# Performance work log

Hardware: AMD Instinct MI355X
Metric: run time of the kernel (lower is better)

Reference implementation:

```python
import jax, jax.numpy as jnp
import numpy as np

V, D, L, H, T_BLK, DFF = 50257, 768, 12, 12, 1024, 4096
DK = D // H
LN_EPS = 1e-5


def setup_inputs() -> dict:
    key = jax.random.key(0)
    ks = jax.random.split(key, 16)
    s = 0.02
    inp = {
        "idx": jax.random.randint(ks[0], (2, 1024), 0, V),
        "tok_emb": jax.random.normal(ks[1], (V, D), jnp.float32) * s,
        "pos_emb": jax.random.normal(ks[2], (1, T_BLK, D), jnp.float32) * s,
        "ln1_w": jnp.ones((L, D), jnp.float32),
        "ln1_b": jnp.zeros((L, D), jnp.float32),
        "qkv_w": jax.random.normal(ks[3], (L, 3 * D, D), jnp.float32) * s,
        "qkv_b": jnp.zeros((L, 3 * D), jnp.float32),
        "proj_w": jax.random.normal(ks[4], (L, D, D), jnp.float32) * s,
        "proj_b": jnp.zeros((L, D), jnp.float32),
        "ln2_w": jnp.ones((L, D), jnp.float32),
        "ln2_b": jnp.zeros((L, D), jnp.float32),
        "ff1_w": jax.random.normal(ks[5], (L, DFF, D), jnp.float32) * s,
        "ff1_b": jnp.zeros((L, DFF), jnp.float32),
        "ff2_w": jax.random.normal(ks[6], (L, D, DFF), jnp.float32) * s,
        "ff2_b": jnp.zeros((L, D), jnp.float32),
        "lnf_w": jnp.ones((D,), jnp.float32),
        "lnf_b": jnp.zeros((D,), jnp.float32),
        "head_w": jax.random.normal(ks[7], (V, D), jnp.float32) * s,
    }
    return inp


def _layernorm(x, w, b):
    mu = jnp.mean(x, axis=-1, keepdims=True)
    var = jnp.var(x, axis=-1, keepdims=True)
    return (x - mu) * jax.lax.rsqrt(var + LN_EPS) * w + b


def _gpt_forward(idx, tok_emb, pos_emb, ln1_w, ln1_b, qkv_w, qkv_b, proj_w, proj_b,
                 ln2_w, ln2_b, ff1_w, ff1_b, ff2_w, ff2_b, lnf_w, lnf_b, head_w):
    B, T = idx.shape
    x = tok_emb[idx] + pos_emb[:, :T, :]  # [B,T,D]
    mask = jnp.tril(jnp.ones((T, T), bool))  # causal
    scale = 1.0 / np.sqrt(DK)

    def step(x, p):
        l1w, l1b, qw, qb, pw, pb, l2w, l2b, f1w, f1b, f2w, f2b = p
        h = _layernorm(x, l1w, l1b)
        qkv = h @ qw.T + qb  # [B,T,3D]
        q, k, v = jnp.split(qkv, 3, axis=-1)
        q = q.reshape(B, T, H, DK).transpose(0, 2, 1, 3)  # [B,H,T,DK]
        k = k.reshape(B, T, H, DK).transpose(0, 2, 1, 3)
        v = v.reshape(B, T, H, DK).transpose(0, 2, 1, 3)
        att = jnp.einsum('bhtd,bhsd->bhts', q, k) * scale
        att = jnp.where(mask, att, -jnp.inf)
        att = jax.nn.softmax(att, axis=-1)
        y = jnp.einsum('bhts,bhsd->bhtd', att, v)
        y = y.transpose(0, 2, 1, 3).reshape(B, T, D)
        x = x + y @ pw.T + pb
        h2 = _layernorm(x, l2w, l2b)
        ff = jax.nn.gelu(h2 @ f1w.T + f1b, approximate=False) @ f2w.T + f2b
        return x + ff, None

    params = (ln1_w, ln1_b, qkv_w, qkv_b, proj_w, proj_b,
              ln2_w, ln2_b, ff1_w, ff1_b, ff2_w, ff2_b)
    x, _ = jax.lax.scan(step, x, params)
    x = _layernorm(x, lnf_w, lnf_b)
    return x @ head_w.T  # [B,T,V] logits


def reference(idx, tok_emb, pos_emb, ln1_w, ln1_b, qkv_w, qkv_b, proj_w, proj_b,
              ln2_w, ln2_b, ff1_w, ff1_b, ff2_w, ff2_b, lnf_w, lnf_b, head_w):
    return _gpt_forward(idx, tok_emb, pos_emb, ln1_w, ln1_b, qkv_w, qkv_b, proj_w,
                        proj_b, ln2_w, ln2_b, ff1_w, ff1_b, ff2_w, ff2_b,
                        lnf_w, lnf_b, head_w)
```

## Files before the change

### kernel.cpp

```cpp
#include <hip/hip_runtime.h>
#include <hip/hip_bf16.h>
#include <math.h>

#define Dm 768
#define Tt 1024
#define Bb 2
#define Hh 12
#define DFF 4096
#define Ll 12
#define Vv 50257
#define ROWS (Bb*Tt)
#define LN_EPS 1e-5f

typedef unsigned int uint;
typedef unsigned short ushort;
typedef float f32x4 __attribute__((ext_vector_type(4)));
typedef short bf16x8 __attribute__((ext_vector_type(8)));
typedef ushort us8 __attribute__((ext_vector_type(8)));

__device__ __forceinline__ ushort f2bf(float f) {
  uint u = __builtin_bit_cast(uint, f);
  u += 0x7FFFu + ((u >> 16) & 1u);
  return (ushort)(u >> 16);
}

#define GLL(gp, lp)                                                          \
  __builtin_amdgcn_global_load_lds(                                          \
      (const __attribute__((address_space(1))) uint*)(gp),                   \
      (__attribute__((address_space(3))) uint*)(lp), 16, 0, 0)

#define MF(a, b, c) __builtin_amdgcn_mfma_f32_16x16x32_bf16(a, b, c, 0, 0, 0)

__global__ __launch_bounds__(256) void embed_ln(
    const int* __restrict__ idx, const float* __restrict__ tok,
    const float* __restrict__ pos, const float* __restrict__ w,
    const float* __restrict__ b, float* __restrict__ x,
    ushort* __restrict__ out) {
  const int row = blockIdx.x;
  const int t = row & (Tt - 1);
  const int tid = threadIdx.x;
  const float* tsrc = tok + (size_t)idx[row] * Dm;
  const float* psrc = pos + (size_t)t * Dm;
  float v[3];
  float sum = 0.f, sq = 0.f;
#pragma unroll
  for (int i = 0; i < 3; i++) {
    const int d = tid + i * 256;
    v[i] = tsrc[d] + psrc[d];
    x[(size_t)row * Dm + d] = v[i];
    sum += v[i]; sq += v[i] * v[i];
  }
#pragma unroll
  for (int off = 32; off > 0; off >>= 1) {
    sum += __shfl_xor(sum, off);
    sq  += __shfl_xor(sq, off);
  }
  __shared__ float red[8];
  const int wid = tid >> 6, lane = tid & 63;
  if (lane == 0) { red[wid] = sum; red[wid + 4] = sq; }
  __syncthreads();
  sum = red[0] + red[1] + red[2] + red[3];
  sq  = red[4] + red[5] + red[6] + red[7];
  const float mu = sum * (1.f / Dm);
  const float var = sq * (1.f / Dm) - mu * mu;
  const float rstd = rsqrtf(var + LN_EPS);
  ushort* dst = out + (size_t)row * Dm;
#pragma unroll
  for (int i = 0; i < 3; i++) {
    const int d = tid + i * 256;
    dst[d] = f2bf((v[i] - mu) * rstd * w[d] + b[d]);
  }
}

__global__ __launch_bounds__(192) void red_ln(
    const float* __restrict__ part, int nsk, const float* __restrict__ bias,
    float* __restrict__ x, const float* __restrict__ w,
    const float* __restrict__ b, ushort* __restrict__ out) {
  const int row = blockIdx.x;
  const int tid = threadIdx.x;
  const size_t o4 = (size_t)row * 192 + tid;
  float4 xv = ((const float4*)x)[o4];
  const float4 b4 = ((const float4*)bias)[tid];
  xv.x += b4.x; xv.y += b4.y; xv.z += b4.z; xv.w += b4.w;
  for (int k = 0; k < nsk; k++) {
    const float4 p = ((const float4*)part)[(size_t)k * ROWS * 192 + o4];
    xv.x += p.x; xv.y += p.y; xv.z += p.z; xv.w += p.w;
  }
  ((float4*)x)[o4] = xv;
  float sum = xv.x + xv.y + xv.z + xv.w;
  float sq = xv.x * xv.x + xv.y * xv.y + xv.z * xv.z + xv.w * xv.w;
#pragma unroll
  for (int off = 32; off > 0; off >>= 1) {
    sum += __shfl_xor(sum, off);
    sq  += __shfl_xor(sq, off);
  }
  __shared__ float red[6];
  const int wid = tid >> 6, lane = tid & 63;
  if (lane == 0) { red[wid] = sum; red[wid + 3] = sq; }
  __syncthreads();
  sum = red[0] + red[1] + red[2];
  sq  = red[3] + red[4] + red[5];
  const float mu = sum * (1.f / Dm);
  const float var = sq * (1.f / Dm) - mu * mu;
  const float rstd = rsqrtf(var + LN_EPS);
  const float4 w4 = ((const float4*)w)[tid];
  const float4 bb4 = ((const float4*)b)[tid];
  ushort4 o;
  o.x = f2bf((xv.x - mu) * rstd * w4.x + bb4.x);
  o.y = f2bf((xv.y - mu) * rstd * w4.y + bb4.y);
  o.z = f2bf((xv.z - mu) * rstd * w4.z + bb4.z);
  o.w = f2bf((xv.w - mu) * rstd * w4.w + bb4.w);
  ((ushort4*)out)[o4] = o;
}

__global__ __launch_bounds__(256) void convert_w(
    const float* __restrict__ s, ushort* __restrict__ d, int n4) {
  const int stride = gridDim.x * 256;
  for (int i = blockIdx.x * 256 + threadIdx.x; i < n4; i += stride) {
    const float4 v = ((const float4*)s)[i];
    ushort4 o;
    o.x = f2bf(v.x); o.y = f2bf(v.y); o.z = f2bf(v.z); o.w = f2bf(v.w);
    ((ushort4*)d)[i] = o;
  }
}

#define EPI_QKV 0
#define EPI_PART 1
#define EPI_BIAS_GELU 2
#define EPI_NONE 3

template <int EPI>
__global__ __launch_bounds__(256) void gemm_mfma(
    const ushort* __restrict__ A, const ushort* __restrict__ B,
    const float* __restrict__ bias, void* __restrict__ Cv,
    void* __restrict__ Cv2, int Kloop, int Kstr, int Nloc, int ldC) {
  __shared__ char lds[32768];
  const int tid = threadIdx.x;
  const int l = tid & 63;
  const int wid = __builtin_amdgcn_readfirstlane(tid >> 6);
  const int wr = wid >> 1, wc = wid & 1;
  const int m0 = blockIdx.y * 128;
  const int n0 = blockIdx.x * 128;
  const int z = (EPI == EPI_PART) ? blockIdx.z : 0;
  if (EPI == EPI_PART) { A += (size_t)z * Kloop; B += (size_t)z * Kloop; }

  const int cperm = (((l & 3) ^ ((l >> 3) & 3)) * 8);
  const ushort* gA = A + (size_t)(m0 + wid * 32 + (l >> 2)) * Kstr + cperm;
  int rB = n0 + wid * 32 + (l >> 2);
  rB = min(rB, Nloc - 1);
  const ushort* gB = B + (size_t)rB * Kstr + cperm;

  const int rdSw = (l & 15) * 64 + (((l >> 4) ^ ((l >> 1) & 3)) * 16);
  const int aRd = wr * 4096 + rdSw;
  const int bRd = 8192 + wc * 4096 + rdSw;

  f32x4 acc[4][4] = {};
  const int nt = Kloop / 32;

  {
    const int lb = wid * 2048;
    GLL(gA, lds + lb);          GLL(gA + 16 * Kstr, lds + lb + 1024);
    GLL(gB, lds + 8192 + lb);   GLL(gB + 16 * Kstr, lds + 8192 + lb + 1024);
  }

  for (int t = 0; t < nt; ++t) {
    __syncthreads();
    if (t + 1 < nt) {
      const int base = ((t + 1) & 1) * 16384;
      const int lb = base + wid * 2048;
      const ushort* a = gA + (t + 1) * 32;
      const ushort* b = gB + (t + 1) * 32;
      GLL(a, lds + lb);         GLL(a + 16 * Kstr, lds + lb + 1024);
      GLL(b, lds + 8192 + lb);  GLL(b + 16 * Kstr, lds + 8192 + lb + 1024);
    }
    const int base = (t & 1) * 16384;
    bf16x8 av[4], bv[4];
#pragma unroll
    for (int i = 0; i < 4; ++i) {
      av[i] = *(const bf16x8*)(lds + base + aRd + i * 1024);
      bv[i] = *(const bf16x8*)(lds + base + bRd + i * 1024);
    }
#pragma unroll
    for (int i = 0; i < 4; ++i)
#pragma unroll
      for (int j = 0; j < 4; ++j)
        acc[i][j] = MF(av[i], bv[j], acc[i][j]);
  }

#pragma unroll
  for (int fm = 0; fm < 4; ++fm) {
    const int row0 = m0 + wr * 64 + fm * 16 + (l >> 4) * 4;
#pragma unroll
    for (int fn = 0; fn < 4; ++fn) {
      const int col = n0 + wc * 64 + fn * 16 + (l & 15);
      if (col >= Nloc) continue;
      float bi = 0.f;
      if (EPI == EPI_QKV || EPI == EPI_BIAS_GELU) bi = bias[col];
      if (EPI == EPI_QKV && col >= 2 * Dm) {
        const int hh = (col - 2 * Dm) >> 6, dd = col & 63;
        const int bI = row0 >> 10, t0 = row0 & (Tt - 1);
        ushort4 o4;
        o4.x = f2bf(acc[fm][fn][0] + bi);
        o4.y = f2bf(acc[fm][fn][1] + bi);
        o4.z = f2bf(acc[fm][fn][2] + bi);
        o4.w = f2bf(acc[fm][fn][3] + bi);
        *(ushort4*)((ushort*)Cv2 +
                    ((size_t)((bI * Hh + hh) * 64 + dd)) * Tt + t0) = o4;
        continue;
      }
#pragma unroll
      for (int r = 0; r < 4; ++r) {
        float v = acc[fm][fn][r] + bi;
        const size_t off = (size_t)(row0 + r) * ldC + col;
        if (EPI == EPI_BIAS_GELU) {
          v = 0.5f * v * (1.f + erff(v * 0.70710678118654752f));
          ((ushort*)Cv)[off] = f2bf(v);
        } else if (EPI == EPI_QKV) {
          ((ushort*)Cv)[off] = f2bf(v);
        } else if (EPI == EPI_PART) {
          ((float*)Cv)[(size_t)z * ROWS * ldC + off] = v;
        } else {
          ((float*)Cv)[off] = v;
        }
      }
    }
  }
}

__global__ __launch_bounds__(512, 2) void gemm_head8(
    const ushort* __restrict__ A, const ushort* __restrict__ B,
    float* __restrict__ C) {
  __shared__ char lds[131072];
  const int tid = threadIdx.x;
  const int l = tid & 63;
  const int wid = __builtin_amdgcn_readfirstlane(tid >> 6);
  const int wm = wid >> 2, wn = wid & 3;
  const int s = l & 15, g = l >> 4;

  const int bid = blockIdx.x;
  const int swz = (bid & 7) * 197 + (bid >> 3);
  const int pan = swz >> 3, mrw = swz & 7;
  const int m0 = mrw * 256;
  const int n0 = pan * 256;

  const int r0 = tid >> 3;
  const int q0 = (tid & 7) ^ (r0 & 7);
  const ushort* pA0 = A + (size_t)(m0 + r0) * Dm + q0 * 8;
  const ushort* pA1 = pA0 + (size_t)64 * Dm;
  const ushort* pB[2][2];
  pB[0][0] = B + (size_t)min(n0 + r0, Vv - 1) * Dm + q0 * 8;
  pB[0][1] = B + (size_t)min(n0 + 64 + r0, Vv - 1) * Dm + q0 * 8;
  pB[1][0] = B + (size_t)min(n0 + 128 + r0, Vv - 1) * Dm + q0 * 8;
  pB[1][1] = B + (size_t)min(n0 + 192 + r0, Vv - 1) * Dm + q0 * 8;

#define STG_A(t, h) do { if ((t) < 12) {                                     \
    char* _d = lds + ((((t) & 1) * 2 + (h)) * 16384);                        \
    GLL(pA0 + (size_t)(h) * 98304 + (t) * 64, _d + tid * 16);                \
    GLL(pA1 + (size_t)(h) * 98304 + (t) * 64, _d + 8192 + tid * 16);         \
  }} while (0)
#define STG_B(t, h) do { if ((t) < 12) {                                     \
    char* _d = lds + 65536 + ((((t) & 1) * 2 + (h)) * 16384);                \
    GLL(pB[h][0] + (t) * 64, _d + tid * 16);                                 \
    GLL(pB[h][1] + (t) * 64, _d + 8192 + tid * 16);                          \
  }} while (0)

  const int aK0 = ((0 * 4 + g) ^ (s & 7)) * 16;
  const int aK1 = ((1 * 4 + g) ^ (s & 7)) * 16;
  const int aBase = wm * 16384 + s * 128;
  const int bBase = 65536 + (wn >> 1) * 16384 + (wn & 1) * 8192 + s * 128;

  f32x4 acc[8][4] = {};
  bf16x8 bv[4][2];

#define PH(t, p, STAGES, VMC)                                                \
  {                                                                          \
    const int cur = ((t) & 1) * 32768;                                       \
    if ((p) == 1) {                                                          \
      _Pragma("unroll")                                                      \
      for (int fn = 0; fn < 4; fn++) {                                       \
        bv[fn][0] = *(const bf16x8*)(lds + cur + bBase + fn * 2048 + aK0);   \
        bv[fn][1] = *(const bf16x8*)(lds + cur + bBase + fn * 2048 + aK1);   \
      }                                                                      \
    }                                                                        \
    bf16x8 a00 = *(const bf16x8*)(lds + cur + aBase + (2*(p)-2)*2048 + aK0); \
    bf16x8 a01 = *(const bf16x8*)(lds + cur + aBase + (2*(p)-2)*2048 + aK1); \
    bf16x8 a10 = *(const bf16x8*)(lds + cur + aBase + (2*(p)-1)*2048 + aK0); \
    bf16x8 a11 = *(const bf16x8*)(lds + cur + aBase + (2*(p)-1)*2048 + aK1); \
    STAGES;                                                                  \
    __builtin_amdgcn_s_barrier();                                            \
    asm volatile("s_waitcnt lgkmcnt(0)" ::: "memory");                       \
    __builtin_amdgcn_sched_barrier(0);                                       \
    __builtin_amdgcn_s_setprio(1);                                           \
    _Pragma("unroll")                                                        \
    for (int fn = 0; fn < 4; fn++) {                                         \
      acc[2*(p)-2][fn] = MF(a00, bv[fn][0], acc[2*(p)-2][fn]);               \
      acc[2*(p)-2][fn] = MF(a01, bv[fn][1], acc[2*(p)-2][fn]);               \
      acc[2*(p)-1][fn] = MF(a10, bv[fn][0], acc[2*(p)-1][fn]);               \
      acc[2*(p)-1][fn] = MF(a11, bv[fn][1], acc[2*(p)-1][fn]);               \
    }                                                                        \
    __builtin_amdgcn_s_setprio(0);                                           \
    VMC;                                                                     \
    __builtin_amdgcn_s_barrier();                                            \
  }

  STG_B(0, 0); STG_B(0, 1); STG_A(0, 0); STG_A(0, 1); STG_B(1, 0); STG_B(1, 1);
  asm volatile("s_waitcnt vmcnt(4)" ::: "memory");
  __builtin_amdgcn_s_barrier();

#pragma unroll 1
  for (int i = 0; i < 6; ++i) {
    const int t0 = 2 * i, t1 = 2 * i + 1, t2 = 2 * i + 2, t3 = 2 * i + 3;
    PH(t0, 1, { STG_A(t1, 0); }, {});
    PH(t0, 2, { STG_A(t1, 1); STG_B(t2, 0); }, {});
    PH(t0, 3, { STG_B(t2, 1); }, {});
    if (i < 5) {
      PH(t0, 4, {}, { asm volatile("s_waitcnt vmcnt(4)" ::: "memory"); });
    } else {
      PH(t0, 4, {}, { asm volatile("s_waitcnt vmcnt(0)" ::: "memory"); });
    }
    PH(t1, 1, { STG_A(t2, 0); }, {});
    PH(t1, 2, { STG_A(t2, 1); }, {});
    PH(t1, 3, { STG_B(t3, 0); }, {});
    if (i < 5) {
      PH(t1, 4, { STG_B(t3, 1); },
         { asm volatile("s_waitcnt vmcnt(4)" ::: "memory"); });
    } else {
      PH(t1, 4, {}, {});
    }
  }

#pragma unroll
  for (int fm = 0; fm < 8; ++fm) {
    const int row0 = m0 + wm * 128 + fm * 16 + g * 4;
#pragma unroll
    for (int fn = 0; fn < 4; ++fn) {
      const int col = n0 + wn * 64 + fn * 16 + s;
      if (col >= Vv) continue;
#pragma unroll
      for (int r = 0; r < 4; ++r)
        C[(size_t)(row0 + r) * Vv + col] = acc[fm][fn][r];
    }
  }
#undef PH
#undef STG_A
#undef STG_B
}

__global__ __launch_bounds__(128) void attn_mfma(
    const ushort* __restrict__ qkv, const ushort* __restrict__ vTg,
    ushort* __restrict__ y) {
  __shared__ char lds[36864];
  const int tid = threadIdx.x;
  const int l = tid & 63;
  const int w = tid >> 6;
  const int s = l & 15, g = l >> 4;
  const int bq = gridDim.x - 1 - blockIdx.x;
  const int h = blockIdx.y, b = blockIdx.z;
  const int bh = b * Hh + h;

  const int qrow = bq * 32 + w * 16 + s;
  const ushort* qp = qkv + (size_t)(b * Tt + qrow) * 2304 + h * 64 + g * 8;
  const bf16x8 aq0 = *(const bf16x8*)qp;
  const bf16x8 aq1 = *(const bf16x8*)(qp + 32);

  size_t gofs[8];
#pragma unroll
  for (int i = 0; i < 8; i++) {
    const int c = tid + i * 128;
    if (i < 4) {
      const int kr = c >> 3;
      gofs[i] = (size_t)(b * Tt + kr) * 2304 + Dm + h * 64 + ((c & 7) ^ (kr & 7)) * 8;
    } else {
      const int cv = c - 512;
      const int vr = cv >> 3;
      gofs[i] = (size_t)(bh * 64 + vr) * Tt + ((cv & 7) ^ (vr & 7)) * 8;
    }
  }

#define ASTAGE(kt, base)                                                     \
  do {                                                                       \
    _Pragma("unroll")                                                        \
    for (int i = 0; i < 8; i++) {                                            \
      const ushort* p = (i < 4) ? (qkv + gofs[i] + (size_t)(kt) * 147456)    \
                                : (vTg + gofs[i] + (kt) * 64);               \
      GLL(p, lds + (base) + tid * 16 + i * 2048);                            \
    }                                                                        \
  } while (0)

  f32x4 oc[4] = {};
  float mrun[4], lrun[4];
#pragma unroll
  for (int r = 0; r < 4; r++) { mrun[r] = -INFINITY; lrun[r] = 0.f; }

  const int pB = 32768 + w * 2048;
  const int kSw = (s & 7);
  const int nkt = (bq >> 1) + 1;

  ASTAGE(0, 0);
  for (int kt = 0; kt < nkt; ++kt) {
    __syncthreads();
    if (kt + 1 < nkt) ASTAGE(kt + 1, ((kt + 1) & 1) * 16384);
    const int cur = (kt & 1) * 16384;

    f32x4 sc[4];
    __builtin_amdgcn_s_setprio(1);
#pragma unroll
    for (int jn = 0; jn < 4; jn++) {
      const int krow = cur + (jn * 16 + s) * 128;
      const bf16x8 bk0 = *(const bf16x8*)(lds + krow + ((g ^ kSw) * 16));
      const bf16x8 bk1 = *(const bf16x8*)(lds + krow + (((4 + g) ^ kSw) * 16));
      f32x4 z = {};
      z = MF(aq0, bk0, z);
      z = MF(aq1, bk1, z);
      sc[jn] = z;
    }
    __builtin_amdgcn_s_setprio(0);

    float cr[4];
    const bool diag = (kt == nkt - 1);
#pragma unroll
    for (int r = 0; r < 4; r++) {
      const int rowg = bq * 32 + w * 16 + g * 4 + r;
      float v[4];
#pragma unroll
      for (int jn = 0; jn < 4; jn++) {
        v[jn] = sc[jn][r] * 0.125f;
        if (diag && (kt * 64 + jn * 16 + s) > rowg) v[jn] = -INFINITY;
      }
      float mx = fmaxf(fmaxf(v[0], v[1]), fmaxf(v[2], v[3]));
      mx = fmaxf(mx, __shfl_xor(mx, 1));
      mx = fmaxf(mx, __shfl_xor(mx, 2));
      mx = fmaxf(mx, __shfl_xor(mx, 4));
      mx = fmaxf(mx, __shfl_xor(mx, 8));
      const float mnew = fmaxf(mrun[r], mx);
      const float corr = __expf(mrun[r] - mnew);
      mrun[r] = mnew;
      float ps = 0.f;
#pragma unroll
      for (int jn = 0; jn < 4; jn++) {
        const float p = __expf(v[jn] - mnew);
        ps += p;
        *(ushort*)(lds + pB + (g * 4 + r) * 128 +
                   (((2 * jn + (s >> 3)) ^ g) * 16) + (s & 7) * 2) = f2bf(p);
      }
      ps += __shfl_xor(ps, 1);
      ps += __shfl_xor(ps, 2);
      ps += __shfl_xor(ps, 4);
      ps += __shfl_xor(ps, 8);
      lrun[r] = lrun[r] * corr + ps;
      cr[r] = corr;
    }

    const float c01 = (s & 1) ? cr[1] : cr[0];
    const float c23 = (s & 1) ? cr[3] : cr[2];
    const float csel = (s & 2) ? c23 : c01;
    const float ccol = __shfl(csel, ((s >> 2) << 4) | s);
#pragma unroll
    for (int fm = 0; fm < 4; fm++) {
      oc[fm][0] *= ccol; oc[fm][1] *= ccol;
      oc[fm][2] *= ccol; oc[fm][3] *= ccol;
    }

    const bf16x8 bp0 = *(const bf16x8*)(lds + pB + s * 128 + ((g ^ (s >> 2)) * 16));
    const bf16x8 bp1 = *(const bf16x8*)(lds + pB + s * 128 + (((4 + g) ^ (s >> 2)) * 16));
    __builtin_amdgcn_s_setprio(1);
#pragma unroll
    for (int fm = 0; fm < 4; fm++) {
      const int vrow = cur + 8192 + (fm * 16 + s) * 128;
      const bf16x8 av0 = *(const bf16x8*)(lds + vrow + ((g ^ kSw) * 16));
      const bf16x8 av1 = *(const bf16x8*)(lds + vrow + (((4 + g) ^ kSw) * 16));
      oc[fm] = MF(av0, bp0, oc[fm]);
      oc[fm] = MF(av1, bp1, oc[fm]);
    }
    __builtin_amdgcn_s_setprio(0);
  }

  float li[4];
#pragma unroll
  for (int r = 0; r < 4; r++) li[r] = 1.f / lrun[r];
  const float l01 = (s & 1) ? li[1] : li[0];
  const float l23 = (s & 1) ? li[3] : li[2];
  const float lsel = (s & 2) ? l23 : l01;
  const float lcol = __shfl(lsel, ((s >> 2) << 4) | s);
  ushort* yp = y + (size_t)(b * Tt + qrow) * Dm + h * 64;
#pragma unroll
  for (int fm = 0; fm < 4; fm++) {
    ushort4 o4;
    o4.x = f2bf(oc[fm][0] * lcol);
    o4.y = f2bf(oc[fm][1] * lcol);
    o4.z = f2bf(oc[fm][2] * lcol);
    o4.w = f2bf(oc[fm][3] * lcol);
    *(ushort4*)(yp + fm * 16 + g * 4) = o4;
  }
}

extern "C" void kernel_launch(void* const* d_in, const int* in_sizes, int n_in,
                              void* d_out, int out_size, void* d_ws, size_t ws_size,
                              hipStream_t stream) {
  const int* idx = (const int*)d_in[0];
  const float* tok = (const float*)d_in[1];
  const float* pos = (const float*)d_in[2];
  const float* ln1w = (const float*)d_in[3];
  const float* ln1b = (const float*)d_in[4];
  const float* qkvw = (const float*)d_in[5];
  const float* qkvb = (const float*)d_in[6];
  const float* projw = (const float*)d_in[7];
  const float* projb = (const float*)d_in[8];
  const float* ln2w = (const float*)d_in[9];
  const float* ln2b = (const float*)d_in[10];
  const float* ff1w = (const float*)d_in[11];
  const float* ff1b = (const float*)d_in[12];
  const float* ff2w = (const float*)d_in[13];
  const float* ff2b = (const float*)d_in[14];
  const float* lnfw = (const float*)d_in[15];
  const float* lnfb = (const float*)d_in[16];
  const float* headw = (const float*)d_in[17];
  float* out = (float*)d_out;

  char* ws = (char*)d_ws;
  ushort* h    = (ushort*)ws;
  float*  x    = (float*)(ws + 3145728);
  ushort* y    = (ushort*)(ws + 9437184);
  ushort* qkv  = (ushort*)(ws + 12582912);
  ushort* vTg  = (ushort*)(ws + 22020096);
  ushort* ff   = (ushort*)(ws + 25165824);
  ushort* wb   = (ushort*)(ws + 41943040);
  float* projPart = (float*)(ws + 326755840);
  float* ff2Part  = (float*)(ws + 351921664);

  const size_t oPROJ = (size_t)Ll * 3 * Dm * Dm;
  const size_t oFF1  = oPROJ + (size_t)Ll * Dm * Dm;
  const size_t oFF2  = oFF1 + (size_t)Ll * DFF * Dm;
  const size_t oHEAD = oFF2 + (size_t)Ll * Dm * DFF;

  convert_w<<<2048, 256, 0, stream>>>(qkvw, wb, (int)(oPROJ / 4));
  convert_w<<<2048, 256, 0, stream>>>(projw, wb + oPROJ, (int)((oFF1 - oPROJ) / 4));
  convert_w<<<2048, 256, 0, stream>>>(ff1w, wb + oFF1, (int)((oFF2 - oFF1) / 4));
  convert_w<<<2048, 256, 0, stream>>>(ff2w, wb + oFF2, (int)((oHEAD - oFF2) / 4));
  convert_w<<<2048, 256, 0, stream>>>(headw, wb + oHEAD, (int)((size_t)Vv * Dm / 4));

  embed_ln<<<ROWS, 256, 0, stream>>>(idx, tok, pos, ln1w, ln1b, x, h);

  for (int l = 0; l < Ll; l++) {
    gemm_mfma<EPI_QKV><<<dim3(18, 16), 256, 0, stream>>>(
        h, wb + (size_t)l * 3 * Dm * Dm, qkvb + l * 3 * Dm, qkv, vTg,
        Dm, Dm, 3 * Dm, 3 * Dm);
    attn_mfma<<<dim3(32, Hh, Bb), 128, 0, stream>>>(qkv, vTg, y);
    gemm_mfma<EPI_PART><<<dim3(6, 16, 4), 256, 0, stream>>>(
        y, wb + oPROJ + (size_t)l * Dm * Dm, nullptr, projPart, nullptr,
        Dm / 4, Dm, Dm, Dm);
    red_ln<<<ROWS, 192, 0, stream>>>(projPart, 4, projb + l * Dm, x,
                                     ln2w + l * Dm, ln2b + l * Dm, h);
    gemm_mfma<EPI_BIAS_GELU><<<dim3(32, 16), 256, 0, stream>>>(
        h, wb + oFF1 + (size_t)l * DFF * Dm, ff1b + l * DFF, ff, nullptr,
        Dm, Dm, DFF, DFF);
    gemm_mfma<EPI_PART><<<dim3(6, 16, 4), 256, 0, stream>>>(
        ff, wb + oFF2 + (size_t)l * Dm * DFF, nullptr, ff2Part, nullptr,
        DFF / 4, DFF, Dm, Dm);
    const float* nw = (l == Ll - 1) ? lnfw : ln1w + (l + 1) * Dm;
    const float* nb = (l == Ll - 1) ? lnfb : ln1b + (l + 1) * Dm;
    red_ln<<<ROWS, 192, 0, stream>>>(ff2Part, 4, ff2b + l * Dm, x, nw, nb, h);
  }

  gemm_head8<<<1576, 512, 0, stream>>>(h, wb + oHEAD, out);
}
```

Before: 2.055 ms.

## Load attention K/V fragments directly from global and merge weight conversions

The attention kernel stops staging K and V tiles into shared memory with asynchronous global-to-LDS loads and double buffering. Each lane now reads its K and V MFMA fragments straight from global memory, which removes the block barrier and shrinks LDS to the P buffer only, allowing more blocks per CU. The cost is uncoalesced, strided global reads that are no longer prefetched. Separately, the five weight fp32-to-bf16 conversion launches are merged into one kernel that picks its source by index range.

New measurement: 2.173 ms. +5.7%, slower.

```diff
diff --git a/kernel.cpp b/kernel.cpp
--- a/kernel.cpp
+++ b/kernel.cpp
@@ -113,14 +113,28 @@
   ((ushort4*)out)[o4] = o;
 }
 
-__global__ __launch_bounds__(256) void convert_w(
-    const float* __restrict__ s, ushort* __restrict__ d, int n4) {
+#define C1 5308416
+#define C2 7077888
+#define C3 16515072
+#define C4 25952256
+#define NALL4 35601600
+
+__global__ __launch_bounds__(256) void convert_all(
+    const float* __restrict__ q, const float* __restrict__ p,
+    const float* __restrict__ f1, const float* __restrict__ f2,
+    const float* __restrict__ hd, ushort* __restrict__ wb) {
   const int stride = gridDim.x * 256;
-  for (int i = blockIdx.x * 256 + threadIdx.x; i < n4; i += stride) {
-    const float4 v = ((const float4*)s)[i];
+  for (int i = blockIdx.x * 256 + threadIdx.x; i < NALL4; i += stride) {
+    const float* s; int j;
+    if (i < C1) { s = q; j = i; }
+    else if (i < C2) { s = p; j = i - C1; }
+    else if (i < C3) { s = f1; j = i - C2; }
+    else if (i < C4) { s = f2; j = i - C3; }
+    else { s = hd; j = i - C4; }
+    const float4 v = ((const float4*)s)[j];
     ushort4 o;
     o.x = f2bf(v.x); o.y = f2bf(v.y); o.z = f2bf(v.z); o.w = f2bf(v.w);
-    ((ushort4*)d)[i] = o;
+    ((ushort4*)wb)[i] = o;
   }
 }
 
@@ -349,7 +363,7 @@
 __global__ __launch_bounds__(128) void attn_mfma(
     const ushort* __restrict__ qkv, const ushort* __restrict__ vTg,
     ushort* __restrict__ y) {
-  __shared__ char lds[36864];
+  __shared__ char lds[4096];
   const int tid = threadIdx.x;
   const int l = tid & 63;
   const int w = tid >> 6;
@@ -363,58 +377,43 @@
   const bf16x8 aq0 = *(const bf16x8*)qp;
   const bf16x8 aq1 = *(const bf16x8*)(qp + 32);
 
-  size_t gofs[8];
-#pragma unroll
-  for (int i = 0; i < 8; i++) {
-    const int c = tid + i * 128;
-    if (i < 4) {
-      const int kr = c >> 3;
-      gofs[i] = (size_t)(b * Tt + kr) * 2304 + Dm + h * 64 + ((c & 7) ^ (kr & 7)) * 8;
-    } else {
-      const int cv = c - 512;
-      const int vr = cv >> 3;
-      gofs[i] = (size_t)(bh * 64 + vr) * Tt + ((cv & 7) ^ (vr & 7)) * 8;
-    }
-  }
-
-#define ASTAGE(kt, base)                                                     \
-  do {                                                                       \
-    _Pragma("unroll")                                                        \
-    for (int i = 0; i < 8; i++) {                                            \
-      const ushort* p = (i < 4) ? (qkv + gofs[i] + (size_t)(kt) * 147456)    \
-                                : (vTg + gofs[i] + (kt) * 64);               \
-      GLL(p, lds + (base) + tid * 16 + i * 2048);                            \
-    }                                                                        \
-  } while (0)
+  const ushort* Kb = qkv + (size_t)(b * Tt) * 2304 + Dm + h * 64 + g * 8;
+  const ushort* Vb = vTg + (size_t)(bh * 64 + s) * Tt + g * 8;
 
   f32x4 oc[4] = {};
   float mrun[4], lrun[4];
 #pragma unroll
   for (int r = 0; r < 4; r++) { mrun[r] = -INFINITY; lrun[r] = 0.f; }
 
-  const int pB = 32768 + w * 2048;
-  const int kSw = (s & 7);
+  const int pB = w * 2048;
   const int nkt = (bq >> 1) + 1;
 
-  ASTAGE(0, 0);
   for (int kt = 0; kt < nkt; ++kt) {
-    __syncthreads();
-    if (kt + 1 < nkt) ASTAGE(kt + 1, ((kt + 1) & 1) * 16384);
-    const int cur = (kt & 1) * 16384;
-
+    bf16x8 bk[4][2];
+#pragma unroll
+    for (int jn = 0; jn < 4; jn++) {
+      const ushort* kp = Kb + (size_t)(kt * 64 + jn * 16 + s) * 2304;
+      bk[jn][0] = *(const bf16x8*)kp;
+      bk[jn][1] = *(const bf16x8*)(kp + 32);
+    }
     f32x4 sc[4];
     __builtin_amdgcn_s_setprio(1);
 #pragma unroll
     for (int jn = 0; jn < 4; jn++) {
-      const int krow = cur + (jn * 16 + s) * 128;
-      const bf16x8 bk0 = *(const bf16x8*)(lds + krow + ((g ^ kSw) * 16));
-      const bf16x8 bk1 = *(const bf16x8*)(lds + krow + (((4 + g) ^ kSw) * 16));
       f32x4 z = {};
-      z = MF(aq0, bk0, z);
-      z = MF(aq1, bk1, z);
+      z = MF(aq0, bk[jn][0], z);
+      z = MF(aq1, bk[jn][1], z);
       sc[jn] = z;
     }
     __builtin_amdgcn_s_setprio(0);
+
+    bf16x8 av[4][2];
+#pragma unroll
+    for (int fm = 0; fm < 4; fm++) {
+      const ushort* vp = Vb + (size_t)(fm * 16) * Tt + kt * 64;
+      av[fm][0] = *(const bf16x8*)vp;
+      av[fm][1] = *(const bf16x8*)(vp + 32);
+    }
 
     float cr[4];
     const bool diag = (kt == nkt - 1);
@@ -466,11 +465,8 @@
     __builtin_amdgcn_s_setprio(1);
 #pragma unroll
     for (int fm = 0; fm < 4; fm++) {
-      const int vrow = cur + 8192 + (fm * 16 + s) * 128;
-      const bf16x8 av0 = *(const bf16x8*)(lds + vrow + ((g ^ kSw) * 16));
-      const bf16x8 av1 = *(const bf16x8*)(lds + vrow + (((4 + g) ^ kSw) * 16));
-      oc[fm] = MF(av0, bp0, oc[fm]);
-      oc[fm] = MF(av1, bp1, oc[fm]);
+      oc[fm] = MF(av[fm][0], bp0, oc[fm]);
+      oc[fm] = MF(av[fm][1], bp1, oc[fm]);
     }
     __builtin_amdgcn_s_setprio(0);
   }
@@ -533,11 +529,7 @@
   const size_t oFF2  = oFF1 + (size_t)Ll * DFF * Dm;
   const size_t oHEAD = oFF2 + (size_t)Ll * Dm * DFF;
 
-  convert_w<<<2048, 256, 0, stream>>>(qkvw, wb, (int)(oPROJ / 4));
-  convert_w<<<2048, 256, 0, stream>>>(projw, wb + oPROJ, (int)((oFF1 - oPROJ) / 4));
-  convert_w<<<2048, 256, 0, stream>>>(ff1w, wb + oFF1, (int)((oFF2 - oFF1) / 4));
-  convert_w<<<2048, 256, 0, stream>>>(ff2w, wb + oFF2, (int)((oHEAD - oFF2) / 4));
-  convert_w<<<2048, 256, 0, stream>>>(headw, wb + oHEAD, (int)((size_t)Vv * Dm / 4));
+  convert_all<<<4096, 256, 0, stream>>>(qkvw, projw, ff1w, ff2w, headw, wb);
 
   embed_ln<<<ROWS, 256, 0, stream>>>(idx, tok, pos, ln1w, ln1b, x, h);
 
```
